# Kernel tuning notes

Hardware: AMD Instinct MI355X
Metric: run time of the kernel (lower is better)

## Reference

```python
import jax, jax.numpy as jnp
import numpy as np

MARGIN = 0.3
EPS = 1e-12

def setup_inputs() -> dict:
    key = jax.random.key(0)
    k1, k2 = jax.random.split(key)
    B, D, NUM_IDS = 1024, 2048, 256
    features = jax.random.normal(k1, (B, D), dtype=jnp.float32)
    labels = jax.random.randint(k2, (B,), 0, NUM_IDS, dtype=jnp.int64)
    return {"features": features, "labels": labels}

def _pairwise_euclidean(features):
    # dist^2 = |x_i|^2 + |x_j|^2 - 2 x_i . x_j, clamped then sqrt (as in torch ref)
    sq = jnp.sum(features * features, axis=1)  # [B]
    d2 = sq[:, None] + sq[None, :] - 2.0 * (features @ features.T)
    return jnp.sqrt(jnp.maximum(d2, EPS))

def reference(features, labels):
    B = features.shape[0]
    dist = _pairwise_euclidean(features)  # [B, B]
    eq = labels[None, :] == labels[:, None]  # [B, B]; eq[i] == labels_equal row i
    eye = jnp.eye(B, dtype=bool)
    pos_mask = eq & ~eye
    neg_mask = ~eq
    neg_inf = jnp.float32(-jnp.inf)
    pos_inf = jnp.float32(jnp.inf)
    hardest_pos = jnp.max(jnp.where(pos_mask, dist, neg_inf), axis=1)  # [B]
    hardest_neg = jnp.min(jnp.where(neg_mask, dist, pos_inf), axis=1)  # [B]
    valid = jnp.any(pos_mask, axis=1) & jnp.any(neg_mask, axis=1)  # rows contributing a triplet
    per_row = jax.nn.relu(hardest_pos - hardest_neg + MARGIN)
    per_row = jnp.where(valid, per_row, 0.0)
    n_valid = jnp.sum(valid)
    loss = jnp.sum(per_row) / jnp.maximum(n_valid, 1).astype(per_row.dtype)
    num_active = jnp.sum(valid & (per_row > 0))
    return loss, num_active
```

## Files before the change

### kernel.cpp

```cpp
#include <hip/hip_runtime.h>
#include <math.h>

#define B_SZ 1024
#define D_SZ 2048
#define MARGIN 0.3f

typedef _Float16 f16x8 __attribute__((ext_vector_type(8)));
typedef float f32x16 __attribute__((ext_vector_type(16)));

union H8 { _Float16 h[8]; uint4 u; };


__global__ __launch_bounds__(256) void sq_kernel(const float* __restrict__ F,
                                                 float* __restrict__ sq) {
    int row = blockIdx.x;
    const float4* r4 = (const float4*)(F + (size_t)row * D_SZ);
    int t = threadIdx.x;
    float s = 0.f;
#pragma unroll
    for (int q = 0; q < 2; ++q) {
        float4 v = r4[t + q * 256];
        s += v.x * v.x + v.y * v.y + v.z * v.z + v.w * v.w;
    }
    for (int off = 32; off; off >>= 1) s += __shfl_down(s, off);
    __shared__ float wsum[4];
    if ((t & 63) == 0) wsum[t >> 6] = s;
    __syncthreads();
    if (t == 0) sq[row] = wsum[0] + wsum[1] + wsum[2] + wsum[3];
}

__global__ __launch_bounds__(256) void init_kernel(int* __restrict__ hp,
                                                   int* __restrict__ hn,
                                                   int* __restrict__ flags) {
    int i = blockIdx.x * 256 + threadIdx.x;
    hp[i] = 0;
    hn[i] = 0x7F800000;
    flags[i] = 0;
}

__global__ __launch_bounds__(1024) void final_kernel(const int* __restrict__ hp,
                                                     const int* __restrict__ hn,
                                                     const int* __restrict__ flags,
                                                     float* __restrict__ out) {
    __shared__ float ssum[16];
    __shared__ int svalid[16], sact[16];
    const int t = threadIdx.x;
    const float hpv = __int_as_float(hp[t]);
    const float hnv = __int_as_float(hn[t]);
    const int f = flags[t];
    const bool valid = (f == 3);
    float pr = fmaxf(hpv - hnv + MARGIN, 0.f);
    if (!valid) pr = 0.f;
    int act = (valid && pr > 0.f) ? 1 : 0;
    int vld = valid ? 1 : 0;
    float s = pr;
    for (int off = 32; off; off >>= 1) {
        s += __shfl_down(s, off);
        act += __shfl_down(act, off);
        vld += __shfl_down(vld, off);
    }
    if ((t & 63) == 0) {
        ssum[t >> 6] = s;
        svalid[t >> 6] = vld;
        sact[t >> 6] = act;
    }
    __syncthreads();
    if (t == 0) {
        float tot = 0.f;
        int nv = 0, na = 0;
#pragma unroll
        for (int i = 0; i < 16; ++i) {
            tot += ssum[i];
            nv += svalid[i];
            na += sact[i];
        }
        out[0] = tot / (float)(nv > 1 ? nv : 1);
        out[1] = (float)na;
    }
}


__global__ __launch_bounds__(256) void prep_f16_kernel(const float* __restrict__ F,
                                                       _Float16* __restrict__ Fh) {
    const int gid = blockIdx.x * 256 + threadIdx.x;
    const int lane = gid & 63;
    const int rg = (gid >> 6) & 1;
    const int kb16 = (gid >> 7) & 127;
    const int i = gid >> 14;
    const int row = i * 64 + rg * 32 + (lane & 31);
    const int k = kb16 * 16 + (lane >> 5) * 8;
    const float4* s = (const float4*)(F + (size_t)row * D_SZ + k);
    const float4 x0 = s[0];
    const float4 x1 = s[1];
    H8 p;
    p.h[0] = (_Float16)x0.x; p.h[1] = (_Float16)x0.y;
    p.h[2] = (_Float16)x0.z; p.h[3] = (_Float16)x0.w;
    p.h[4] = (_Float16)x1.x; p.h[5] = (_Float16)x1.y;
    p.h[6] = (_Float16)x1.z; p.h[7] = (_Float16)x1.w;
    *(uint4*)(Fh + (size_t)gid * 8) = p.u;
}

#define WAVE_STAGE (3 * 8192)

__global__ __launch_bounds__(256) void dist_f16_kernel(
    const _Float16* __restrict__ Fh, const int* __restrict__ labels,
    const float* __restrict__ sq, int* __restrict__ hp, int* __restrict__ hn,
    int* __restrict__ flags) {
    __shared__ __align__(16) char stage[4 * WAVE_STAGE];
    __shared__ int labR[64], labC[64];
    __shared__ float sqR[64], sqC[64];

    const int t = threadIdx.x;
    const int lane = t & 63;
    const int w = t >> 6;

    const int tileId = (blockIdx.x & 7) * 32 + (blockIdx.x >> 3);
    const int bi = tileId >> 4;
    const int bj = tileId & 15;
    const int rowBase = bi * 64, colBase = bj * 64;

    if (t < 64) {
        labR[t] = labels[rowBase + t];
        sqR[t] = sq[rowBase + t];
    } else if (t < 128) {
        int u = t - 64;
        labC[u] = labels[colBase + u];
        sqC[u] = sq[colBase + u];
    }
    asm volatile("s_waitcnt vmcnt(0)" ::: "memory");

    const char* FhB = (const char*)Fh;
    char* wbase = stage + w * WAVE_STAGE;
    const char* rbase = wbase + lane * 16;

    f32x16 acc[2][2];
#pragma unroll
    for (int a = 0; a < 2; ++a)
#pragma unroll
        for (int c = 0; c < 2; ++c)
#pragma unroll
            for (int e = 0; e < 16; ++e) acc[a][c][e] = 0.f;

    auto ISSUE = [&](int s, int b) {
        const int kb16 = w * 32 + s * 2;
        const size_t aOff = (size_t)((bi * 128 + kb16) * 2) * 1024 + (size_t)lane * 16;
        const size_t bOff = (size_t)((bj * 128 + kb16) * 2) * 1024 + (size_t)lane * 16;
        char* dA = wbase + b * 8192;
#pragma unroll
        for (int c = 0; c < 4; ++c)
            __builtin_amdgcn_global_load_lds(
                (const __attribute__((address_space(1))) void*)(FhB + aOff + c * 1024),
                (__attribute__((address_space(3))) void*)(dA + c * 1024), 16, 0, 0);
#pragma unroll
        for (int c = 0; c < 4; ++c)
            __builtin_amdgcn_global_load_lds(
                (const __attribute__((address_space(1))) void*)(FhB + bOff + c * 1024),
                (__attribute__((address_space(3))) void*)(dA + 4096 + c * 1024), 16, 0, 0);
    };
    auto COMPUTE = [&](int b) {
        const char* rb = rbase + b * 8192;
#pragma unroll
        for (int kl = 0; kl < 2; ++kl) {
            f16x8 a0 = *(const f16x8*)(rb + (kl * 2 + 0) * 1024);
            f16x8 a1 = *(const f16x8*)(rb + (kl * 2 + 1) * 1024);
            f16x8 v0 = *(const f16x8*)(rb + 4096 + (kl * 2 + 0) * 1024);
            f16x8 v1 = *(const f16x8*)(rb + 4096 + (kl * 2 + 1) * 1024);
            acc[0][0] = __builtin_amdgcn_mfma_f32_32x32x16_f16(a0, v0, acc[0][0], 0, 0, 0);
            acc[0][1] = __builtin_amdgcn_mfma_f32_32x32x16_f16(a0, v1, acc[0][1], 0, 0, 0);
            acc[1][0] = __builtin_amdgcn_mfma_f32_32x32x16_f16(a1, v0, acc[1][0], 0, 0, 0);
            acc[1][1] = __builtin_amdgcn_mfma_f32_32x32x16_f16(a1, v1, acc[1][1], 0, 0, 0);
        }
    };

#define WAIT16 asm volatile("s_waitcnt vmcnt(16)" ::: "memory"); __builtin_amdgcn_sched_barrier(0)
#define WAIT8  asm volatile("s_waitcnt vmcnt(8)"  ::: "memory"); __builtin_amdgcn_sched_barrier(0)
#define WAIT0  asm volatile("s_waitcnt vmcnt(0)"  ::: "memory"); __builtin_amdgcn_sched_barrier(0)

    ISSUE(0, 0);
    ISSUE(1, 1);
    for (int s3 = 0; s3 < 12; s3 += 3) {
        ISSUE(s3 + 2, 2); WAIT16; COMPUTE(0);
        ISSUE(s3 + 3, 0); WAIT16; COMPUTE(1);
        ISSUE(s3 + 4, 1); WAIT16; COMPUTE(2);
    }
    ISSUE(14, 2); WAIT16; COMPUTE(0);
    ISSUE(15, 0); WAIT16; COMPUTE(1);
    WAIT8;  COMPUTE(2);
    WAIT0;  COMPUTE(0);

    __syncthreads();

    char* cb = stage;
#pragma unroll
    for (int fr = 0; fr < 2; ++fr)
#pragma unroll
        for (int fc = 0; fc < 2; ++fc)
#pragma unroll
            for (int g = 0; g < 4; ++g) {
                float4 v;
                v.x = acc[fr][fc][g * 4 + 0];
                v.y = acc[fr][fc][g * 4 + 1];
                v.z = acc[fr][fc][g * 4 + 2];
                v.w = acc[fr][fc][g * 4 + 3];
                *(float4*)(cb + ((size_t)((w * 16 + (fr * 2 + fc) * 4 + g) * 64 + lane)) * 16) = v;
            }
    __syncthreads();

    const int fr = w >> 1, fc = w & 1;
    float cS[16];
#pragma unroll
    for (int e = 0; e < 16; ++e) cS[e] = 0.f;
#pragma unroll
    for (int wp = 0; wp < 4; ++wp)
#pragma unroll
        for (int g = 0; g < 4; ++g) {
            float4 v = *(const float4*)(cb + ((size_t)((wp * 16 + w * 4 + g) * 64 + lane)) * 16);
            cS[g * 4 + 0] += v.x;
            cS[g * 4 + 1] += v.y;
            cS[g * 4 + 2] += v.z;
            cS[g * 4 + 3] += v.w;
        }

    const float BIG = 1e38f;
    const int h = lane >> 5;
    const int colL = fc * 32 + (lane & 31);
    const int j = colBase + colL;
    const int lj = labC[colL];
    const float sqj = sqC[colL];
#pragma unroll
    for (int k = 0; k < 16; ++k) {
        const int rowL = fr * 32 + (k & 3) + 8 * (k >> 2) + 4 * h;
        const int i = rowBase + rowL;
        const float d2 = sqR[rowL] + sqj - 2.f * cS[k];
        const float d = sqrtf(fmaxf(d2, 1e-12f));
        const bool eq = (labR[rowL] == lj);
        const bool isPos = eq && (i != j);
        float pv = isPos ? d : -BIG;
        float nv = eq ? BIG : d;
        int pf = (isPos ? 1 : 0) | (eq ? 0 : 2);
#pragma unroll
        for (int mask = 1; mask < 32; mask <<= 1) {
            pv = fmaxf(pv, __shfl_xor(pv, mask));
            nv = fminf(nv, __shfl_xor(nv, mask));
            pf |= __shfl_xor(pf, mask);
        }
        if ((lane & 31) == 0) {
            if (pf & 1) atomicMax(&hp[i], __float_as_int(pv));
            if (pf & 2) atomicMin(&hn[i], __float_as_int(nv));
            if (pf) atomicOr(&flags[i], pf);
        }
    }
}


#define BM 64
#define BN 64
#define BK 32

__global__ __launch_bounds__(256) void dist_f32_kernel(
    const float* __restrict__ F, const int* __restrict__ labels,
    const float* __restrict__ sq, int* __restrict__ hp, int* __restrict__ hn,
    int* __restrict__ flags) {
    __shared__ float As[BK][BM];
    __shared__ float Bs[BK][BN];
    __shared__ int labR[BM], labC[BN];
    __shared__ float sqR[BM], sqC[BN];

    const int rowBase = blockIdx.y * BM;
    const int colBase = blockIdx.x * BN;
    const int t = threadIdx.x;
    const int tx = t & 15;
    const int ty = t >> 4;

    if (t < 64) {
        labR[t] = labels[rowBase + t];
        sqR[t] = sq[rowBase + t];
    } else if (t < 128) {
        int u = t - 64;
        labC[u] = labels[colBase + u];
        sqC[u] = sq[colBase + u];
    }

    float acc[4][4] = {{0.f}};
    const int m = t & 63;
    const int q = t >> 6;
    const float* aRow = F + (size_t)(rowBase + m) * D_SZ + q * 8;
    const float* bRow = F + (size_t)(colBase + m) * D_SZ + q * 8;

    for (int k0 = 0; k0 < D_SZ; k0 += BK) {
        float4 a0 = *(const float4*)(aRow + k0);
        float4 a1 = *(const float4*)(aRow + k0 + 4);
        float4 b0 = *(const float4*)(bRow + k0);
        float4 b1 = *(const float4*)(bRow + k0 + 4);
        __syncthreads();
        int kb = q * 8;
        As[kb + 0][m] = a0.x; As[kb + 1][m] = a0.y;
        As[kb + 2][m] = a0.z; As[kb + 3][m] = a0.w;
        As[kb + 4][m] = a1.x; As[kb + 5][m] = a1.y;
        As[kb + 6][m] = a1.z; As[kb + 7][m] = a1.w;
        Bs[kb + 0][m] = b0.x; Bs[kb + 1][m] = b0.y;
        Bs[kb + 2][m] = b0.z; Bs[kb + 3][m] = b0.w;
        Bs[kb + 4][m] = b1.x; Bs[kb + 5][m] = b1.y;
        Bs[kb + 6][m] = b1.z; Bs[kb + 7][m] = b1.w;
        __syncthreads();
#pragma unroll
        for (int kk = 0; kk < BK; ++kk) {
            float4 a = *(const float4*)&As[kk][ty * 4];
            float4 b = *(const float4*)&Bs[kk][tx * 4];
            acc[0][0] += a.x * b.x; acc[0][1] += a.x * b.y;
            acc[0][2] += a.x * b.z; acc[0][3] += a.x * b.w;
            acc[1][0] += a.y * b.x; acc[1][1] += a.y * b.y;
            acc[1][2] += a.y * b.z; acc[1][3] += a.y * b.w;
            acc[2][0] += a.z * b.x; acc[2][1] += a.z * b.y;
            acc[2][2] += a.z * b.z; acc[2][3] += a.z * b.w;
            acc[3][0] += a.w * b.x; acc[3][1] += a.w * b.y;
            acc[3][2] += a.w * b.z; acc[3][3] += a.w * b.w;
        }
    }

    float mp[4], mn[4];
    int pf[4];
#pragma unroll
    for (int rr = 0; rr < 4; ++rr) {
        const int i = rowBase + ty * 4 + rr;
        const int li = labR[ty * 4 + rr];
        const float si = sqR[ty * 4 + rr];
        mp[rr] = -3.4e38f;
        mn[rr] = 3.4e38f;
        pf[rr] = 0;
#pragma unroll
        for (int c = 0; c < 4; ++c) {
            const int j = colBase + tx * 4 + c;
            const float d2 = si + sqC[tx * 4 + c] - 2.f * acc[rr][c];
            const float dist = sqrtf(fmaxf(d2, 1e-12f));
            const bool eq = (li == labC[tx * 4 + c]);
            if (eq && (i != j)) {
                mp[rr] = fmaxf(mp[rr], dist);
                pf[rr] |= 1;
            }
            if (!eq) {
                mn[rr] = fminf(mn[rr], dist);
                pf[rr] |= 2;
            }
        }
    }
#pragma unroll
    for (int mask = 1; mask < 16; mask <<= 1)
#pragma unroll
        for (int rr = 0; rr < 4; ++rr) {
            mp[rr] = fmaxf(mp[rr], __shfl_xor(mp[rr], mask));
            mn[rr] = fminf(mn[rr], __shfl_xor(mn[rr], mask));
            pf[rr] |= __shfl_xor(pf[rr], mask);
        }
    if (tx == 0) {
#pragma unroll
        for (int rr = 0; rr < 4; ++rr) {
            const int i = rowBase + ty * 4 + rr;
            if (pf[rr] & 1) atomicMax(&hp[i], __float_as_int(mp[rr]));
            if (pf[rr] & 2) atomicMin(&hn[i], __float_as_int(mn[rr]));
            if (pf[rr]) atomicOr(&flags[i], pf[rr]);
        }
    }
}


extern "C" void kernel_launch(void* const* d_in, const int* in_sizes, int n_in,
                              void* d_out, int out_size, void* d_ws, size_t ws_size,
                              hipStream_t stream) {
    const float* F = (const float*)d_in[0];
    const int* labels = (const int*)d_in[1];
    float* out = (float*)d_out;
    char* ws = (char*)d_ws;

    const size_t FH = (size_t)B_SZ * D_SZ * 2;
    const size_t need = FH + 16 * 1024;

    if (ws_size >= need) {
        _Float16* Fh = (_Float16*)ws;
        char* tail = ws + FH;
        float* sq = (float*)tail;
        int* hp = (int*)(tail + 4096);
        int* hn = (int*)(tail + 8192);
        int* flags = (int*)(tail + 12288);

        prep_f16_kernel<<<(B_SZ * D_SZ) / (256 * 8), 256, 0, stream>>>(F, Fh);
        sq_kernel<<<B_SZ, 256, 0, stream>>>(F, sq);
        init_kernel<<<B_SZ / 256, 256, 0, stream>>>(hp, hn, flags);
        dist_f16_kernel<<<256, 256, 0, stream>>>(Fh, labels, sq, hp, hn, flags);
        final_kernel<<<1, 1024, 0, stream>>>(hp, hn, flags, out);
    } else {
        float* sq = (float*)ws;
        int* hp = (int*)(ws + 4096);
        int* hn = (int*)(ws + 8192);
        int* flags = (int*)(ws + 12288);

        sq_kernel<<<B_SZ, 256, 0, stream>>>(F, sq);
        init_kernel<<<B_SZ / 256, 256, 0, stream>>>(hp, hn, flags);
        dim3 grid(B_SZ / BN, B_SZ / BM);
        dist_f32_kernel<<<grid, 256, 0, stream>>>(F, labels, sq, hp, hn, flags);
        final_kernel<<<1, 1024, 0, stream>>>(hp, hn, flags, out);
    }
}
```

Measured before the change: 33.20 us.

## Fuse f16 conversion, row norms and init into one prep kernel; load fragments via registers

Merges the f16 conversion, squared-norm computation and accumulator init into a single prep kernel that reads F once, writing per-segment partial norms that the distance kernel sums. This removes two kernel launches and a second full read of F. The distance kernel now loads MFMA fragments straight from global memory into registers with a triple-buffered register pipeline, replacing the LDS-staged async loads and explicit waitcnt scheduling. The register buffers raise VGPR pressure, and the staging through LDS in prep adds a transpose step.

```diff
diff --git a/kernel.cpp b/kernel.cpp
--- a/kernel.cpp
+++ b/kernel.cpp
@@ -8,35 +8,212 @@
 typedef _Float16 f16x8 __attribute__((ext_vector_type(8)));
 typedef float f32x16 __attribute__((ext_vector_type(16)));
 
-union H8 { _Float16 h[8]; uint4 u; };
-
-
-__global__ __launch_bounds__(256) void sq_kernel(const float* __restrict__ F,
-                                                 float* __restrict__ sq) {
-    int row = blockIdx.x;
-    const float4* r4 = (const float4*)(F + (size_t)row * D_SZ);
-    int t = threadIdx.x;
-    float s = 0.f;
-#pragma unroll
-    for (int q = 0; q < 2; ++q) {
-        float4 v = r4[t + q * 256];
-        s += v.x * v.x + v.y * v.y + v.z * v.z + v.w * v.w;
-    }
-    for (int off = 32; off; off >>= 1) s += __shfl_down(s, off);
-    __shared__ float wsum[4];
-    if ((t & 63) == 0) wsum[t >> 6] = s;
-    __syncthreads();
-    if (t == 0) sq[row] = wsum[0] + wsum[1] + wsum[2] + wsum[3];
-}
-
-__global__ __launch_bounds__(256) void init_kernel(int* __restrict__ hp,
+union FragU { uint4 u; f16x8 v; };
+union H4 { _Float16 h[4]; uint2 u; };
+
+
+
+__global__ __launch_bounds__(256) void prep_kernel(const float* __restrict__ F,
+                                                   _Float16* __restrict__ Fh,
+                                                   float* __restrict__ sqpart,
+                                                   int* __restrict__ hp,
                                                    int* __restrict__ hn,
                                                    int* __restrict__ flags) {
-    int i = blockIdx.x * 256 + threadIdx.x;
-    hp[i] = 0;
-    hn[i] = 0x7F800000;
-    flags[i] = 0;
-}
+    __shared__ _Float16 slab[64][136];
+    __shared__ float part[64];
+
+    const int b = blockIdx.x;
+    const int i = b >> 4;
+    const int kseg = b & 15;
+    const int t = threadIdx.x;
+    const int lane = t & 63;
+    const int w = t >> 6;
+
+    const int idx = b * 256 + t;
+    if (idx < 1024) {
+        hp[idx] = 0;
+        hn[idx] = 0x7F800000;
+        flags[idx] = 0;
+    }
+
+#pragma unroll
+    for (int q = 0; q < 8; ++q) {
+        const int rl = q * 8 + (t >> 5);
+        const int c4 = (t & 31) * 4;
+        const float4 v = *(const float4*)(F + (size_t)(i * 64 + rl) * D_SZ +
+                                          kseg * 128 + c4);
+        float s = v.x * v.x + v.y * v.y + v.z * v.z + v.w * v.w;
+#pragma unroll
+        for (int mask = 1; mask < 32; mask <<= 1) s += __shfl_xor(s, mask);
+        if ((t & 31) == 0) part[rl] = s;
+        H4 p;
+        p.h[0] = (_Float16)v.x; p.h[1] = (_Float16)v.y;
+        p.h[2] = (_Float16)v.z; p.h[3] = (_Float16)v.w;
+        *(uint2*)&slab[rl][c4] = p.u;
+    }
+    __syncthreads();
+
+    if (t < 64) sqpart[kseg * 1024 + i * 64 + t] = part[t];
+
+#pragma unroll
+    for (int q2 = 0; q2 < 4; ++q2) {
+        const int u = w * 4 + q2;
+        const int kb = u >> 1;
+        const int rg = u & 1;
+        const uint4 d = *(const uint4*)&slab[rg * 32 + (lane & 31)]
+                                          [kb * 16 + (lane >> 5) * 8];
+        const size_t g = (size_t)((i * 128 + kseg * 8 + kb) * 2 + rg);
+        *(uint4*)((char*)Fh + g * 1024 + (size_t)lane * 16) = d;
+    }
+}
+
+
+__global__ __launch_bounds__(256) void dist_f16_kernel(
+    const _Float16* __restrict__ Fh, const int* __restrict__ labels,
+    const float* __restrict__ sqpart, int* __restrict__ hp,
+    int* __restrict__ hn, int* __restrict__ flags) {
+    __shared__ __align__(16) char comb[65536];
+    __shared__ int labR[64], labC[64];
+    __shared__ float sqR[64], sqC[64];
+
+    const int t = threadIdx.x;
+    const int lane = t & 63;
+    const int w = t >> 6;
+
+    const int tileId = (blockIdx.x & 7) * 32 + (blockIdx.x >> 3);
+    const int bi = tileId >> 4;
+    const int bj = tileId & 15;
+    const int rowBase = bi * 64, colBase = bj * 64;
+
+    if (t < 128) {
+        const int e = t & 63;
+        const int side = t >> 6;
+        const int row = (side ? colBase : rowBase) + e;
+        float s = 0.f;
+#pragma unroll
+        for (int p = 0; p < 16; ++p) s += sqpart[p * 1024 + row];
+        if (side) { sqC[e] = s; labC[e] = labels[row]; }
+        else      { sqR[e] = s; labR[e] = labels[row]; }
+    }
+    __syncthreads();
+
+    const char* __restrict__ FhB = (const char*)Fh;
+
+    f32x16 acc[2][2];
+#pragma unroll
+    for (int a = 0; a < 2; ++a)
+#pragma unroll
+        for (int c = 0; c < 2; ++c)
+#pragma unroll
+            for (int e = 0; e < 16; ++e) acc[a][c][e] = 0.f;
+
+    uint4 A[3][4], Bv[3][4];
+
+#define LOADAB(s, buf)                                                          \
+    {                                                                           \
+        const int kb16 = w * 32 + (s) * 2;                                      \
+        _Pragma("unroll")                                                       \
+        for (int kl = 0; kl < 2; ++kl)                                          \
+            _Pragma("unroll")                                                   \
+            for (int rg = 0; rg < 2; ++rg) {                                    \
+                A[buf][kl * 2 + rg] = *(const uint4*)(FhB +                     \
+                    (size_t)(((bi * 128 + kb16 + kl) * 2 + rg)) * 1024 +        \
+                    (size_t)lane * 16);                                         \
+                Bv[buf][kl * 2 + rg] = *(const uint4*)(FhB +                    \
+                    (size_t)(((bj * 128 + kb16 + kl) * 2 + rg)) * 1024 +        \
+                    (size_t)lane * 16);                                         \
+            }                                                                   \
+    }
+
+#define MFMA8(buf)                                                              \
+    {                                                                           \
+        _Pragma("unroll")                                                       \
+        for (int kl = 0; kl < 2; ++kl) {                                        \
+            FragU a0, a1, v0, v1;                                               \
+            a0.u = A[buf][kl * 2 + 0];                                          \
+            a1.u = A[buf][kl * 2 + 1];                                          \
+            v0.u = Bv[buf][kl * 2 + 0];                                         \
+            v1.u = Bv[buf][kl * 2 + 1];                                         \
+            acc[0][0] = __builtin_amdgcn_mfma_f32_32x32x16_f16(a0.v, v0.v, acc[0][0], 0, 0, 0); \
+            acc[0][1] = __builtin_amdgcn_mfma_f32_32x32x16_f16(a0.v, v1.v, acc[0][1], 0, 0, 0); \
+            acc[1][0] = __builtin_amdgcn_mfma_f32_32x32x16_f16(a1.v, v0.v, acc[1][0], 0, 0, 0); \
+            acc[1][1] = __builtin_amdgcn_mfma_f32_32x32x16_f16(a1.v, v1.v, acc[1][1], 0, 0, 0); \
+        }                                                                       \
+    }
+
+    LOADAB(0, 0);
+    LOADAB(1, 1);
+    LOADAB(2, 2);
+#pragma unroll
+    for (int s = 0; s < 16; ++s) {
+        const int c = s % 3;
+        MFMA8(c);
+        if (s + 3 < 16) LOADAB(s + 3, c);
+    }
+
+#pragma unroll
+    for (int fr = 0; fr < 2; ++fr)
+#pragma unroll
+        for (int fc = 0; fc < 2; ++fc)
+#pragma unroll
+            for (int g = 0; g < 4; ++g) {
+                float4 v;
+                v.x = acc[fr][fc][g * 4 + 0];
+                v.y = acc[fr][fc][g * 4 + 1];
+                v.z = acc[fr][fc][g * 4 + 2];
+                v.w = acc[fr][fc][g * 4 + 3];
+                *(float4*)(comb + ((size_t)((w * 16 + (fr * 2 + fc) * 4 + g) * 64 + lane)) * 16) = v;
+            }
+    __syncthreads();
+
+    const int fr = w >> 1, fc = w & 1;
+    float cS[16];
+#pragma unroll
+    for (int e = 0; e < 16; ++e) cS[e] = 0.f;
+#pragma unroll
+    for (int wp = 0; wp < 4; ++wp)
+#pragma unroll
+        for (int g = 0; g < 4; ++g) {
+            float4 v = *(const float4*)(comb + ((size_t)((wp * 16 + w * 4 + g) * 64 + lane)) * 16);
+            cS[g * 4 + 0] += v.x;
+            cS[g * 4 + 1] += v.y;
+            cS[g * 4 + 2] += v.z;
+            cS[g * 4 + 3] += v.w;
+        }
+
+    const float BIG = 1e38f;
+    const int h = lane >> 5;
+    const int colL = fc * 32 + (lane & 31);
+    const int j = colBase + colL;
+    const int lj = labC[colL];
+    const float sqj = sqC[colL];
+#pragma unroll
+    for (int k = 0; k < 16; ++k) {
+        const int rowL = fr * 32 + (k & 3) + 8 * (k >> 2) + 4 * h;
+        const int i = rowBase + rowL;
+        const float d2 = sqR[rowL] + sqj - 2.f * cS[k];
+        const float d = sqrtf(fmaxf(d2, 1e-12f));
+        const bool eq = (labR[rowL] == lj);
+        const bool isPos = eq && (i != j);
+        float pv = isPos ? d : -BIG;
+        float nv = eq ? BIG : d;
+        int pf = (isPos ? 1 : 0) | (eq ? 0 : 2);
+#pragma unroll
+        for (int mask = 1; mask < 32; mask <<= 1) {
+            pv = fmaxf(pv, __shfl_xor(pv, mask));
+            nv = fminf(nv, __shfl_xor(nv, mask));
+            pf |= __shfl_xor(pf, mask);
+        }
+        if ((lane & 31) == 0) {
+            if (pf & 1) atomicMax(&hp[i], __float_as_int(pv));
+            if (pf & 2) atomicMin(&hn[i], __float_as_int(nv));
+            if (pf) atomicOr(&flags[i], pf);
+        }
+    }
+#undef LOADAB
+#undef MFMA8
+}
+
 
 __global__ __launch_bounds__(1024) void final_kernel(const int* __restrict__ hp,
                                                      const int* __restrict__ hn,
@@ -80,182 +257,36 @@
 }
 
 
-__global__ __launch_bounds__(256) void prep_f16_kernel(const float* __restrict__ F,
-                                                       _Float16* __restrict__ Fh) {
-    const int gid = blockIdx.x * 256 + threadIdx.x;
-    const int lane = gid & 63;
-    const int rg = (gid >> 6) & 1;
-    const int kb16 = (gid >> 7) & 127;
-    const int i = gid >> 14;
-    const int row = i * 64 + rg * 32 + (lane & 31);
-    const int k = kb16 * 16 + (lane >> 5) * 8;
-    const float4* s = (const float4*)(F + (size_t)row * D_SZ + k);
-    const float4 x0 = s[0];
-    const float4 x1 = s[1];
-    H8 p;
-    p.h[0] = (_Float16)x0.x; p.h[1] = (_Float16)x0.y;
-    p.h[2] = (_Float16)x0.z; p.h[3] = (_Float16)x0.w;
-    p.h[4] = (_Float16)x1.x; p.h[5] = (_Float16)x1.y;
-    p.h[6] = (_Float16)x1.z; p.h[7] = (_Float16)x1.w;
-    *(uint4*)(Fh + (size_t)gid * 8) = p.u;
-}
-
-#define WAVE_STAGE (3 * 8192)
-
-__global__ __launch_bounds__(256) void dist_f16_kernel(
-    const _Float16* __restrict__ Fh, const int* __restrict__ labels,
-    const float* __restrict__ sq, int* __restrict__ hp, int* __restrict__ hn,
-    int* __restrict__ flags) {
-    __shared__ __align__(16) char stage[4 * WAVE_STAGE];
-    __shared__ int labR[64], labC[64];
-    __shared__ float sqR[64], sqC[64];
-
-    const int t = threadIdx.x;
-    const int lane = t & 63;
-    const int w = t >> 6;
-
-    const int tileId = (blockIdx.x & 7) * 32 + (blockIdx.x >> 3);
-    const int bi = tileId >> 4;
-    const int bj = tileId & 15;
-    const int rowBase = bi * 64, colBase = bj * 64;
-
-    if (t < 64) {
-        labR[t] = labels[rowBase + t];
-        sqR[t] = sq[rowBase + t];
-    } else if (t < 128) {
-        int u = t - 64;
-        labC[u] = labels[colBase + u];
-        sqC[u] = sq[colBase + u];
-    }
-    asm volatile("s_waitcnt vmcnt(0)" ::: "memory");
-
-    const char* FhB = (const char*)Fh;
-    char* wbase = stage + w * WAVE_STAGE;
-    const char* rbase = wbase + lane * 16;
-
-    f32x16 acc[2][2];
-#pragma unroll
-    for (int a = 0; a < 2; ++a)
-#pragma unroll
-        for (int c = 0; c < 2; ++c)
-#pragma unroll
-            for (int e = 0; e < 16; ++e) acc[a][c][e] = 0.f;
-
-    auto ISSUE = [&](int s, int b) {
-        const int kb16 = w * 32 + s * 2;
-        const size_t aOff = (size_t)((bi * 128 + kb16) * 2) * 1024 + (size_t)lane * 16;
-        const size_t bOff = (size_t)((bj * 128 + kb16) * 2) * 1024 + (size_t)lane * 16;
-        char* dA = wbase + b * 8192;
-#pragma unroll
-        for (int c = 0; c < 4; ++c)
-            __builtin_amdgcn_global_load_lds(
-                (const __attribute__((address_space(1))) void*)(FhB + aOff + c * 1024),
-                (__attribute__((address_space(3))) void*)(dA + c * 1024), 16, 0, 0);
-#pragma unroll
-        for (int c = 0; c < 4; ++c)
-            __builtin_amdgcn_global_load_lds(
-                (const __attribute__((address_space(1))) void*)(FhB + bOff + c * 1024),
-                (__attribute__((address_space(3))) void*)(dA + 4096 + c * 1024), 16, 0, 0);
-    };
-    auto COMPUTE = [&](int b) {
-        const char* rb = rbase + b * 8192;
-#pragma unroll
-        for (int kl = 0; kl < 2; ++kl) {
-            f16x8 a0 = *(const f16x8*)(rb + (kl * 2 + 0) * 1024);
-            f16x8 a1 = *(const f16x8*)(rb + (kl * 2 + 1) * 1024);
-            f16x8 v0 = *(const f16x8*)(rb + 4096 + (kl * 2 + 0) * 1024);
-            f16x8 v1 = *(const f16x8*)(rb + 4096 + (kl * 2 + 1) * 1024);
-            acc[0][0] = __builtin_amdgcn_mfma_f32_32x32x16_f16(a0, v0, acc[0][0], 0, 0, 0);
-            acc[0][1] = __builtin_amdgcn_mfma_f32_32x32x16_f16(a0, v1, acc[0][1], 0, 0, 0);
-            acc[1][0] = __builtin_amdgcn_mfma_f32_32x32x16_f16(a1, v0, acc[1][0], 0, 0, 0);
-            acc[1][1] = __builtin_amdgcn_mfma_f32_32x32x16_f16(a1, v1, acc[1][1], 0, 0, 0);
-        }
-    };
-
-#define WAIT16 asm volatile("s_waitcnt vmcnt(16)" ::: "memory"); __builtin_amdgcn_sched_barrier(0)
-#define WAIT8  asm volatile("s_waitcnt vmcnt(8)"  ::: "memory"); __builtin_amdgcn_sched_barrier(0)
-#define WAIT0  asm volatile("s_waitcnt vmcnt(0)"  ::: "memory"); __builtin_amdgcn_sched_barrier(0)
-
-    ISSUE(0, 0);
-    ISSUE(1, 1);
-    for (int s3 = 0; s3 < 12; s3 += 3) {
-        ISSUE(s3 + 2, 2); WAIT16; COMPUTE(0);
-        ISSUE(s3 + 3, 0); WAIT16; COMPUTE(1);
-        ISSUE(s3 + 4, 1); WAIT16; COMPUTE(2);
-    }
-    ISSUE(14, 2); WAIT16; COMPUTE(0);
-    ISSUE(15, 0); WAIT16; COMPUTE(1);
-    WAIT8;  COMPUTE(2);
-    WAIT0;  COMPUTE(0);
-
-    __syncthreads();
-
-    char* cb = stage;
-#pragma unroll
-    for (int fr = 0; fr < 2; ++fr)
-#pragma unroll
-        for (int fc = 0; fc < 2; ++fc)
-#pragma unroll
-            for (int g = 0; g < 4; ++g) {
-                float4 v;
-                v.x = acc[fr][fc][g * 4 + 0];
-                v.y = acc[fr][fc][g * 4 + 1];
-                v.z = acc[fr][fc][g * 4 + 2];
-                v.w = acc[fr][fc][g * 4 + 3];
-                *(float4*)(cb + ((size_t)((w * 16 + (fr * 2 + fc) * 4 + g) * 64 + lane)) * 16) = v;
-            }
-    __syncthreads();
-
-    const int fr = w >> 1, fc = w & 1;
-    float cS[16];
-#pragma unroll
-    for (int e = 0; e < 16; ++e) cS[e] = 0.f;
-#pragma unroll
-    for (int wp = 0; wp < 4; ++wp)
-#pragma unroll
-        for (int g = 0; g < 4; ++g) {
-            float4 v = *(const float4*)(cb + ((size_t)((wp * 16 + w * 4 + g) * 64 + lane)) * 16);
-            cS[g * 4 + 0] += v.x;
-            cS[g * 4 + 1] += v.y;
-            cS[g * 4 + 2] += v.z;
-            cS[g * 4 + 3] += v.w;
-        }
-
-    const float BIG = 1e38f;
-    const int h = lane >> 5;
-    const int colL = fc * 32 + (lane & 31);
-    const int j = colBase + colL;
-    const int lj = labC[colL];
-    const float sqj = sqC[colL];
-#pragma unroll
-    for (int k = 0; k < 16; ++k) {
-        const int rowL = fr * 32 + (k & 3) + 8 * (k >> 2) + 4 * h;
-        const int i = rowBase + rowL;
-        const float d2 = sqR[rowL] + sqj - 2.f * cS[k];
-        const float d = sqrtf(fmaxf(d2, 1e-12f));
-        const bool eq = (labR[rowL] == lj);
-        const bool isPos = eq && (i != j);
-        float pv = isPos ? d : -BIG;
-        float nv = eq ? BIG : d;
-        int pf = (isPos ? 1 : 0) | (eq ? 0 : 2);
-#pragma unroll
-        for (int mask = 1; mask < 32; mask <<= 1) {
-            pv = fmaxf(pv, __shfl_xor(pv, mask));
-            nv = fminf(nv, __shfl_xor(nv, mask));
-            pf |= __shfl_xor(pf, mask);
-        }
-        if ((lane & 31) == 0) {
-            if (pf & 1) atomicMax(&hp[i], __float_as_int(pv));
-            if (pf & 2) atomicMin(&hn[i], __float_as_int(nv));
-            if (pf) atomicOr(&flags[i], pf);
-        }
-    }
-}
-
-
 #define BM 64
 #define BN 64
 #define BK 32
+
+__global__ __launch_bounds__(256) void sq_kernel(const float* __restrict__ F,
+                                                 float* __restrict__ sq) {
+    int row = blockIdx.x;
+    const float4* r4 = (const float4*)(F + (size_t)row * D_SZ);
+    int t = threadIdx.x;
+    float s = 0.f;
+#pragma unroll
+    for (int q = 0; q < 2; ++q) {
+        float4 v = r4[t + q * 256];
+        s += v.x * v.x + v.y * v.y + v.z * v.z + v.w * v.w;
+    }
+    for (int off = 32; off; off >>= 1) s += __shfl_down(s, off);
+    __shared__ float wsum[4];
+    if ((t & 63) == 0) wsum[t >> 6] = s;
+    __syncthreads();
+    if (t == 0) sq[row] = wsum[0] + wsum[1] + wsum[2] + wsum[3];
+}
+
+__global__ __launch_bounds__(256) void init_kernel(int* __restrict__ hp,
+                                                   int* __restrict__ hn,
+                                                   int* __restrict__ flags) {
+    int i = blockIdx.x * 256 + threadIdx.x;
+    hp[i] = 0;
+    hn[i] = 0x7F800000;
+    flags[i] = 0;
+}
 
 __global__ __launch_bounds__(256) void dist_f32_kernel(
     const float* __restrict__ F, const int* __restrict__ labels,
@@ -373,20 +404,19 @@
     char* ws = (char*)d_ws;
 
     const size_t FH = (size_t)B_SZ * D_SZ * 2;
-    const size_t need = FH + 16 * 1024;
+    const size_t SQP = 16 * 1024 * sizeof(float);
+    const size_t need = FH + SQP + 12 * 1024;
 
     if (ws_size >= need) {
         _Float16* Fh = (_Float16*)ws;
-        char* tail = ws + FH;
-        float* sq = (float*)tail;
-        int* hp = (int*)(tail + 4096);
-        int* hn = (int*)(tail + 8192);
-        int* flags = (int*)(tail + 12288);
-
-        prep_f16_kernel<<<(B_SZ * D_SZ) / (256 * 8), 256, 0, stream>>>(F, Fh);
-        sq_kernel<<<B_SZ, 256, 0, stream>>>(F, sq);
-        init_kernel<<<B_SZ / 256, 256, 0, stream>>>(hp, hn, flags);
-        dist_f16_kernel<<<256, 256, 0, stream>>>(Fh, labels, sq, hp, hn, flags);
+        float* sqpart = (float*)(ws + FH);
+        char* tail = ws + FH + SQP;
+        int* hp = (int*)tail;
+        int* hn = (int*)(tail + 4096);
+        int* flags = (int*)(tail + 8192);
+
+        prep_kernel<<<256, 256, 0, stream>>>(F, Fh, sqpart, hp, hn, flags);
+        dist_f16_kernel<<<256, 256, 0, stream>>>(Fh, labels, sqpart, hp, hn, flags);
         final_kernel<<<1, 1024, 0, stream>>>(hp, hn, flags, out);
     } else {
         float* sq = (float*)ws;
```

After: 37.63 us. +13.3%, slower.
